# Performance work log

Measured on AMD Instinct MI355X. Metric: run time of the kernel, lower is better.

## Reference

```python
import jax, jax.numpy as jnp
import numpy as np

B, C, N = 2, 256, 8192
H = W = 64
C4 = C // 4
EPS = 1e-5


def bn(x, gamma, beta, mean, var):
    # eval-mode batchnorm over channel axis 1
    shape = (1, -1) + (1,) * (x.ndim - 2)
    inv = gamma * jax.lax.rsqrt(var + EPS)
    return x * inv.reshape(shape) + (beta - mean * inv).reshape(shape)


def conv1x1(x, w, b):
    # w: (Cout, Cin)
    return jnp.einsum('bchw,oc->bohw', x, w) + b.reshape(1, -1, 1, 1)


def conv2d(x, w, b=None, padding='VALID', groups=1, lhs_dilation=None):
    y = jax.lax.conv_general_dilated(
        x, w, window_strides=(1, 1), padding=padding,
        lhs_dilation=lhs_dilation, feature_group_count=groups,
        dimension_numbers=('NCHW', 'OIHW', 'NCHW'))
    return y if b is None else y + b.reshape(1, -1, 1, 1)


def lift_net(x, w1, b1, w2, b2, axis):
    # DAWN predictor/updater: ReflectionPad(2,1) -> conv k=4 along axis (C4->2C4)
    # -> ReLU -> 1x1 conv (2C4->C4) -> Tanh
    pad = [(0, 0)] * 4
    pad[axis] = (2, 1)
    xp = jnp.pad(x, pad, mode='reflect')
    k = w1[:, :, None, :] if axis == 3 else w1[:, :, :, None]
    h = jax.nn.relu(conv2d(xp, k, b1))
    return jnp.tanh(conv1x1(h, w2, b2))


def lifting(x, pw, axis):
    # pw = (w1, b1, w2, b2), each with leading net axis [P, U]
    w1, b1, w2, b2 = pw
    sl_e = [slice(None)] * 4; sl_e[axis] = slice(0, None, 2)
    sl_o = [slice(None)] * 4; sl_o[axis] = slice(1, None, 2)
    x_even, x_odd = x[tuple(sl_e)], x[tuple(sl_o)]
    d = x_odd - lift_net(x_even, w1[0], b1[0], w2[0], b2[0], axis)
    c = x_even + lift_net(d, w1[1], b1[1], w2[1], b2[1], axis)
    return c, d


def wavelet2d(x, w1, b1, w2, b2):
    # leading axes of weights: (scheme[horizontal, vertical], net[P, U])
    c, d = lifting(x, (w1[0], b1[0], w2[0], b2[0]), axis=3)  # split along W
    v = (w1[1], b1[1], w2[1], b2[1])                          # shared vertical weights
    LL, LH = lifting(c, v, axis=2)
    HL, HH = lifting(d, v, axis=2)
    return LL, LH, HL, HH


def convT(x, w, b):
    # torch ConvTranspose2d(k=4, stride=2, pad=1); w: (Cin, Cout, 4, 4)
    wc = jnp.flip(w, (2, 3)).transpose(1, 0, 2, 3)  # (Cout, Cin, 4, 4)
    return conv2d(x, wc, b, padding=[(2, 2), (2, 2)], lhs_dilation=(2, 2))


def _forward(tokens, flatten_mat, bn_gamma, bn_beta, bn_mean, bn_var, red_w, red_b,
             lift_w1, lift_b1, lift_w2, lift_b2,
             ff2_w1, ff2_b1, ff2_w2, ff2_b2, ct2_w, ct2_b,
             bn2_gamma, bn2_beta, bn2_mean, bn2_var,
             ff1_w1, ff1_b1, ff1_w2, ff1_b2, ct1_w, ct1_b,
             bn1_gamma, bn1_beta, bn1_mean, bn1_var,
             dw1_w, dw1_b, dw2_w, dw2_b, scale_w, inflate_idx):
    r = bn(tokens, bn_gamma, bn_beta, bn_mean, bn_var)                       # (B,C,N)
    r = jnp.einsum('bmn,bcn->bcm', flatten_mat, r).reshape(B, C, H, W)       # flatten to grid
    rr = conv1x1(r, red_w, red_b)                                            # (B,C/4,H,W)
    LL1, LH1, HL1, HH1 = wavelet2d(rr, lift_w1[0], lift_b1[0], lift_w2[0], lift_b2[0])
    LL2, LH2, HL2, HH2 = wavelet2d(LL1, lift_w1[1], lift_b1[1], lift_w2[1], lift_b2[1])
    x2 = jnp.concatenate([LL2, LH2, HL2, HH2], 1)                            # (B,C,H/4,W/4)
    y2 = conv1x1(jax.nn.gelu(conv1x1(x2, ff2_w1, ff2_b1), approximate=False), ff2_w2, ff2_b2)
    y2 = bn(convT(y2, ct2_w, ct2_b), bn2_gamma, bn2_beta, bn2_mean, bn2_var) # (B,C/2,H/2,W/2)
    x1 = jnp.concatenate([LL1, LH1, HL1, HH1, y2], 1)                        # (B,1.5C,H/2,W/2)
    y1 = conv1x1(jax.nn.gelu(conv1x1(x1, ff1_w1, ff1_b1), approximate=False), ff1_w2, ff1_b2)
    y1 = bn(convT(y1, ct1_w, ct1_b), bn1_gamma, bn1_beta, bn1_mean, bn1_var) # (B,C,H,W)
    r = r + y1
    r = conv2d(r, dw1_w, dw1_b, padding=[(1, 1), (1, 1)], groups=C)          # depthwise 3x3
    r = conv2d(jax.nn.relu(r), dw2_w, dw2_b, padding=[(1, 1), (1, 1)], groups=C)
    r = r.reshape(B, C, H * W) * scale_w.reshape(1, C, 1)                    # grouped 1x1 conv1d
    r = jnp.take_along_axis(r, inflate_idx, axis=2)                          # inflate gather
    return tokens + r


def setup_inputs() -> dict:
    key = jax.random.key(0)
    ks = iter(jax.random.split(key, 64))
    nrm = lambda shape, s=0.05: jax.random.normal(next(ks), shape, jnp.float32) * s
    uni = lambda shape: jax.random.uniform(next(ks), shape, jnp.float32, 0.5, 1.5)
    return dict(
        tokens=jax.random.normal(next(ks), (B, C, N), jnp.float32),
        flatten_mat=nrm((B, H * W, N), 0.02),
        inflate_idx=jax.random.randint(next(ks), (B, C, N), 0, H * W),
        bn_gamma=jnp.ones((C,), jnp.float32), bn_beta=jnp.zeros((C,), jnp.float32),
        bn_mean=nrm((C,), 0.1), bn_var=uni((C,)),
        red_w=nrm((C4, C)), red_b=nrm((C4,)),
        lift_w1=nrm((2, 2, 2, 2 * C4, C4, 4)), lift_b1=nrm((2, 2, 2, 2 * C4)),
        lift_w2=nrm((2, 2, 2, C4, 2 * C4)), lift_b2=nrm((2, 2, 2, C4)),
        ff2_w1=nrm((C, C)), ff2_b1=nrm((C,)), ff2_w2=nrm((C, C)), ff2_b2=nrm((C,)),
        ct2_w=nrm((C, C // 2, 4, 4)), ct2_b=nrm((C // 2,)),
        bn2_gamma=jnp.ones((C // 2,), jnp.float32), bn2_beta=jnp.zeros((C // 2,), jnp.float32),
        bn2_mean=nrm((C // 2,), 0.1), bn2_var=uni((C // 2,)),
        ff1_w1=nrm((C, C + C // 2)), ff1_b1=nrm((C,)), ff1_w2=nrm((C, C)), ff1_b2=nrm((C,)),
        ct1_w=nrm((C, C, 4, 4)), ct1_b=nrm((C,)),
        bn1_gamma=jnp.ones((C,), jnp.float32), bn1_beta=jnp.zeros((C,), jnp.float32),
        bn1_mean=nrm((C,), 0.1), bn1_var=uni((C,)),
        dw1_w=nrm((C, 1, 3, 3)), dw1_b=nrm((C,)),
        dw2_w=nrm((C, 1, 3, 3)), dw2_b=nrm((C,)),
        scale_w=nrm((C,), 0.2),
    )


def reference(tokens, flatten_mat, inflate_idx, bn_gamma, bn_beta, bn_mean, bn_var,
              red_w, red_b, lift_w1, lift_b1, lift_w2, lift_b2,
              ff2_w1, ff2_b1, ff2_w2, ff2_b2, ct2_w, ct2_b,
              bn2_gamma, bn2_beta, bn2_mean, bn2_var,
              ff1_w1, ff1_b1, ff1_w2, ff1_b2, ct1_w, ct1_b,
              bn1_gamma, bn1_beta, bn1_mean, bn1_var,
              dw1_w, dw1_b, dw2_w, dw2_b, scale_w):
    return _forward(tokens, flatten_mat, bn_gamma, bn_beta, bn_mean, bn_var, red_w, red_b,
                    lift_w1, lift_b1, lift_w2, lift_b2,
                    ff2_w1, ff2_b1, ff2_w2, ff2_b2, ct2_w, ct2_b,
                    bn2_gamma, bn2_beta, bn2_mean, bn2_var,
                    ff1_w1, ff1_b1, ff1_w2, ff1_b2, ct1_w, ct1_b,
                    bn1_gamma, bn1_beta, bn1_mean, bn1_var,
                    dw1_w, dw1_b, dw2_w, dw2_b, scale_w, inflate_idx)
```

## Files before the change

kernel.cpp:

```cpp
#include <hip/hip_runtime.h>
#include <math.h>

#define EPSV 1e-5f

typedef __attribute__((ext_vector_type(8))) short bf16x8;
typedef __attribute__((ext_vector_type(4))) float f32x4;
typedef __attribute__((ext_vector_type(8))) unsigned short u16x8;

__device__ inline unsigned short f2bf(float f) {
    unsigned u = __float_as_uint(f);
    unsigned r = (u + 0x7fffu + ((u >> 16) & 1u)) >> 16;
    return (unsigned short)r;
}

__device__ inline void gload_lds16(const void* g, void* l) {
    __builtin_amdgcn_global_load_lds(
        (const __attribute__((address_space(1))) void*)g,
        (__attribute__((address_space(3))) void*)l, 16, 0, 0);
}

__global__ __launch_bounds__(256) void bn_to_bf16_kernel(
    const float4* __restrict__ x, ushort4* __restrict__ y,
    const float* __restrict__ g, const float* __restrict__ be,
    const float* __restrict__ mu, const float* __restrict__ va)
{
    int i = blockIdx.x * 256 + threadIdx.x;
    int c = (i >> 11) & 255;
    float s = g[c] * rsqrtf(va[c] + EPSV);
    float t = be[c] - mu[c] * s;
    float4 v = x[i];
    ushort4 h;
    h.x = f2bf(v.x * s + t); h.y = f2bf(v.y * s + t);
    h.z = f2bf(v.z * s + t); h.w = f2bf(v.w * s + t);
    y[i] = h;
}

__global__ __launch_bounds__(256) void flatten_gemm_mfma(
    const unsigned short* __restrict__ A, const float* __restrict__ Bm,
    float* __restrict__ Pbase)
{
    __shared__ __align__(16) unsigned short AS[4][256 * 32];
    __shared__ __align__(16) unsigned short BS[4][64 * 32];
    const int NTT = 64;
    int t = threadIdx.x;
    int wid = t >> 6, lane = t & 63;
    int n0 = blockIdx.x * 64;
    int ks = blockIdx.z & 3, b = blockIdx.z >> 2;
    const unsigned short* Ab = A + b * (256 * 8192);
    const float* Bb = Bm + (long)b * (4096 * 8192) + (long)n0 * 8192;
    int k0 = ks * 2048;
    int brow = t >> 3, bc8 = t & 7;
    int l15 = lane & 15, kc = lane >> 4;

    f32x4 acc[4][4] = {};

    auto issueA = [&](int tile, int buf) {
        int kb = k0 + tile * 32;
        #pragma unroll
        for (int j = 0; j < 4; ++j) {
            int d16 = (wid * 4 + j) * 64 + lane;
            int row = d16 >> 2;
            int ch = (d16 & 3) ^ ((row >> 1) & 3);
            gload_lds16(Ab + row * 8192 + kb + ch * 8, &AS[buf][(wid * 4 + j) * 512]);
        }
    };
    auto loadB = [&](int tile, float4& f0, float4& f1) {
        int kb = k0 + tile * 32;
        f0 = *(const float4*)(Bb + brow * 8192 + kb + bc8 * 4);
        f1 = *(const float4*)(Bb + (brow + 32) * 8192 + kb + bc8 * 4);
    };
    auto writeB = [&](int buf, const float4& f0, const float4& f1) {
        int ch16 = (bc8 >> 1) ^ ((brow >> 1) & 3);
        ushort4 h;
        h.x = f2bf(f0.x); h.y = f2bf(f0.y); h.z = f2bf(f0.z); h.w = f2bf(f0.w);
        *reinterpret_cast<ushort4*>(&BS[buf][brow * 32 + ch16 * 8 + (bc8 & 1) * 4]) = h;
        int rr2 = brow + 32;
        int ch16b = (bc8 >> 1) ^ ((rr2 >> 1) & 3);
        ushort4 h2;
        h2.x = f2bf(f1.x); h2.y = f2bf(f1.y); h2.z = f2bf(f1.z); h2.w = f2bf(f1.w);
        *reinterpret_cast<ushort4*>(&BS[buf][rr2 * 32 + ch16b * 8 + (bc8 & 1) * 4]) = h2;
    };
    auto mmac = [&](int buf) {
        bf16x8 af[4], bfr[4];
        #pragma unroll
        for (int mf = 0; mf < 4; ++mf) {
            int row = wid * 64 + mf * 16 + l15;
            int ch = kc ^ ((row >> 1) & 3);
            af[mf] = *reinterpret_cast<const bf16x8*>(&AS[buf][row * 32 + ch * 8]);
        }
        #pragma unroll
        for (int nf = 0; nf < 4; ++nf) {
            int row = nf * 16 + l15;
            int ch = kc ^ ((row >> 1) & 3);
            bfr[nf] = *reinterpret_cast<const bf16x8*>(&BS[buf][row * 32 + ch * 8]);
        }
        #pragma unroll
        for (int mf = 0; mf < 4; ++mf)
            #pragma unroll
            for (int nf = 0; nf < 4; ++nf)
                acc[mf][nf] = __builtin_amdgcn_mfma_f32_16x16x32_bf16(
                    af[mf], bfr[nf], acc[mf][nf], 0, 0, 0);
    };

    float4 p0, p1, e0, e1, q0, q1, r0, r1;
    loadB(0, p0, p1);
    loadB(1, e0, e1);
    loadB(2, q0, q1);
    issueA(0, 0); issueA(1, 1); issueA(2, 2);
    writeB(0, p0, p1);
    writeB(1, e0, e1);
    asm volatile("s_waitcnt vmcnt(8) lgkmcnt(0)" ::: "memory");
    __builtin_amdgcn_s_barrier();
    __builtin_amdgcn_sched_barrier(0);

    for (int tau = 0; tau < NTT; ++tau) {
        int cur = tau & 3;
        if (tau + 3 < NTT) {
            loadB(tau + 3, r0, r1);
            issueA(tau + 3, (tau + 3) & 3);
        }
        if (tau + 2 < NTT)
            writeB((tau + 2) & 3, q0, q1);
        mmac(cur);
        if (tau < NTT - 3)
            asm volatile("s_waitcnt vmcnt(8) lgkmcnt(0)" ::: "memory");
        else if (tau == NTT - 3)
            asm volatile("s_waitcnt vmcnt(4) lgkmcnt(0)" ::: "memory");
        else
            asm volatile("s_waitcnt vmcnt(0) lgkmcnt(0)" ::: "memory");
        __builtin_amdgcn_s_barrier();
        __builtin_amdgcn_sched_barrier(0);
        q0 = r0; q1 = r1;
    }

    float* P = Pbase + (long)ks * 2097152;
    float* Cb = P + (b * 256) * 4096 + n0;
    #pragma unroll
    for (int mf = 0; mf < 4; ++mf) {
        int rbase = wid * 64 + mf * 16 + (lane >> 4) * 4;
        #pragma unroll
        for (int nf = 0; nf < 4; ++nf) {
            int col = nf * 16 + (lane & 15);
            #pragma unroll
            for (int r = 0; r < 4; ++r)
                Cb[(rbase + r) * 4096 + col] = acc[mf][nf][r];
        }
    }
}

__global__ __launch_bounds__(256) void add4_t_kernel(
    const float* __restrict__ p, float* __restrict__ of32, unsigned short* __restrict__ obf)
{
    __shared__ float tl[64][65];
    int t = threadIdx.x;
    int b = blockIdx.z;
    int c0 = blockIdx.y * 64, p0 = blockIdx.x * 64;
    #pragma unroll
    for (int u = 0; u < 16; ++u) {
        int idx = u * 256 + t;
        int cl = idx >> 6, pl = idx & 63;
        long g = (long)(b * 256 + c0 + cl) * 4096 + p0 + pl;
        float v = p[g] + p[g + 2097152] + p[g + 2 * 2097152] + p[g + 3 * 2097152];
        tl[cl][pl] = v;
        of32[g] = v;
    }
    __syncthreads();
    #pragma unroll
    for (int u = 0; u < 16; ++u) {
        int idx = u * 256 + t;
        int pl = idx >> 6, cl = idx & 63;
        obf[(long)(b * 4096 + p0 + pl) * 256 + c0 + cl] = f2bf(tl[cl][pl]);
    }
}

__global__ __launch_bounds__(256) void wpack_kernel(
    const float* __restrict__ w, unsigned short* __restrict__ wp, int Cout, int Cin)
{
    int id = blockIdx.x * 256 + threadIdx.x;
    int nc8 = Cin >> 3;
    int cch = id % nc8;
    int rest = id / nc8;
    int o = rest % Cout;
    int pt = rest / Cout;
    if (pt >= 16) return;
    int par = pt >> 2, tap = pt & 3;
    int py = par >> 1, px = par & 1, u = tap >> 1, v = tap & 1;
    int tf = (3 - py - 2 * u) * 4 + (3 - px - 2 * v);
    u16x8 h;
    #pragma unroll
    for (int e = 0; e < 8; ++e)
        h[e] = f2bf(w[((cch * 8 + e) * Cout + o) * 16 + tf]);
    *reinterpret_cast<u16x8*>(&wp[((pt * Cout + o) * Cin) + cch * 8]) = h;
}

template<int NF>
__global__ __launch_bounds__(256) void conv1x1_mfma(
    const unsigned short* __restrict__ xbf, const float* __restrict__ w,
    const float* __restrict__ bias, float* __restrict__ of32,
    unsigned short* __restrict__ obf, int Cin, int Cout, int P, int act)
{
    constexpr int BP = NF * 64;
    __shared__ __align__(16) unsigned short XS[2][BP * 32];
    __shared__ __align__(16) unsigned short WS[2][64 * 32];
    int t = threadIdx.x;
    int wid = t >> 6, lane = t & 63;
    int b = blockIdx.z;
    int p0 = blockIdx.x * BP, o0 = blockIdx.y * 64;
    const unsigned short* xb = xbf + (long)b * P * Cin;
    int wm = t >> 2, wq = t & 3;
    int chunks = Cin >> 5;

    f32x4 acc[4][NF] = {};

    #pragma unroll
    for (int j = 0; j < NF; ++j) {
        int d16 = (wid * NF + j) * 64 + lane;
        int p = d16 >> 2;
        int ch = (d16 & 3) ^ ((p >> 1) & 3);
        gload_lds16(xb + (long)(p0 + p) * Cin + ch * 8, &XS[0][(wid * NF + j) * 512]);
    }
    float4 wr0 = *(const float4*)(w + (o0 + wm) * Cin + wq * 8);
    float4 wr1 = *(const float4*)(w + (o0 + wm) * Cin + wq * 8 + 4);
    __syncthreads();

    for (int cc = 0; cc < chunks; ++cc) {
        int cur = cc & 1;
        {
            int chq = wq ^ ((wm >> 1) & 3);
            u16x8 h;
            h[0] = f2bf(wr0.x); h[1] = f2bf(wr0.y); h[2] = f2bf(wr0.z); h[3] = f2bf(wr0.w);
            h[4] = f2bf(wr1.x); h[5] = f2bf(wr1.y); h[6] = f2bf(wr1.z); h[7] = f2bf(wr1.w);
            *reinterpret_cast<u16x8*>(&WS[cur][wm * 32 + chq * 8]) = h;
        }
        __syncthreads();

        if (cc < chunks - 1) {
            int kn = (cc + 1) * 32;
            #pragma unroll
            for (int j = 0; j < NF; ++j) {
                int d16 = (wid * NF + j) * 64 + lane;
                int p = d16 >> 2;
                int ch = (d16 & 3) ^ ((p >> 1) & 3);
                gload_lds16(xb + (long)(p0 + p) * Cin + kn + ch * 8,
                            &XS[cur ^ 1][(wid * NF + j) * 512]);
            }
            wr0 = *(const float4*)(w + (o0 + wm) * Cin + kn + wq * 8);
            wr1 = *(const float4*)(w + (o0 + wm) * Cin + kn + wq * 8 + 4);
        }

        int l15 = lane & 15, kc = lane >> 4;
        bf16x8 af[4], bfr[NF];
        #pragma unroll
        for (int mf = 0; mf < 4; ++mf) {
            int row = mf * 16 + l15;
            int ch = kc ^ ((row >> 1) & 3);
            af[mf] = *reinterpret_cast<const bf16x8*>(&WS[cur][row * 32 + ch * 8]);
        }
        #pragma unroll
        for (int nf = 0; nf < NF; ++nf) {
            int row = wid * (NF * 16) + nf * 16 + l15;
            int ch = kc ^ ((row >> 1) & 3);
            bfr[nf] = *reinterpret_cast<const bf16x8*>(&XS[cur][row * 32 + ch * 8]);
        }
        #pragma unroll
        for (int mf = 0; mf < 4; ++mf)
            #pragma unroll
            for (int nf = 0; nf < NF; ++nf)
                acc[mf][nf] = __builtin_amdgcn_mfma_f32_16x16x32_bf16(
                    af[mf], bfr[nf], acc[mf][nf], 0, 0, 0);
        __syncthreads();
    }

    int l15 = lane & 15, kc4 = lane >> 4;
    #pragma unroll
    for (int mf = 0; mf < 4; ++mf) {
        #pragma unroll
        for (int nf = 0; nf < NF; ++nf) {
            int p = wid * (NF * 16) + nf * 16 + l15;
            ushort4 hb;
            #pragma unroll
            for (int r = 0; r < 4; ++r) {
                int m = mf * 16 + kc4 * 4 + r;
                float v = acc[mf][nf][r] + bias[o0 + m];
                if (act == 1) v = fmaxf(v, 0.f);
                else if (act == 2) v = 0.5f * v * (1.f + erff(v * 0.70710678118f));
                if (of32) of32[((long)(b * Cout) + o0 + m) * P + p0 + p] = v;
                ((unsigned short*)&hb)[r] = f2bf(v);
            }
            if (obf)
                *reinterpret_cast<ushort4*>(
                    &obf[(long)(b * P + p0 + p) * Cout + o0 + mf * 16 + kc4 * 4]) = hb;
        }
    }
}

__global__ __launch_bounds__(256) void convt_mfma(
    const unsigned short* __restrict__ xbf, const unsigned short* __restrict__ wp,
    const float* __restrict__ bias, const float* __restrict__ g,
    const float* __restrict__ be, const float* __restrict__ mu,
    const float* __restrict__ va, const float* __restrict__ res,
    float* __restrict__ of32, unsigned short* __restrict__ obf,
    int Cin, int Cout, int Hin, int Win, int TR, int cshift, int OCtot, int cof)
{
    __shared__ __align__(16) unsigned short XS[165 * 32];
    __shared__ __align__(16) unsigned short WS[4 * 64 * 32];
    int t = threadIdx.x;
    int wid = t >> 6, lane = t & 63;
    int z = blockIdx.z;
    int b = z >> 2, par = z & 3;
    int py = par >> 1, px = par & 1;
    int o0 = blockIdx.y * 64;
    int i0 = blockIdx.x * TR;
    int CW = Win, CW1 = CW + 1;
    int npatch = (TR + 1) * CW1;
    int Pin = Hin * Win, Pout = 4 * Hin * Win;
    const unsigned short* xb = xbf + (long)b * Pin * Cin;
    int chunks = Cin >> 5;
    int l15 = lane & 15, kc = lane >> 4;

    f32x4 acc[4][2] = {};

    for (int cc = 0; cc < chunks; ++cc) {
        __syncthreads();
        for (int idx = t; idx < npatch * 4; idx += 256) {
            int pp = idx >> 2, ql = idx & 3;
            int qs = ql ^ ((pp >> 1) & 3);
            int a = pp / CW1, bcol = pp - a * CW1;
            int iy = i0 - (1 - py) + a;
            int ix = bcol - (1 - px);
            u16x8 v = {};
            if (iy >= 0 && iy < Hin && ix >= 0 && ix < Win)
                v = *reinterpret_cast<const u16x8*>(
                    &xb[(long)(iy * Win + ix) * Cin + cc * 32 + qs * 8]);
            *reinterpret_cast<u16x8*>(&XS[pp * 32 + ql * 8]) = v;
        }
        {
            int m = t >> 2, q = t & 3;
            int chq = q ^ ((m >> 1) & 3);
            #pragma unroll
            for (int tap = 0; tap < 4; ++tap) {
                u16x8 v = *reinterpret_cast<const u16x8*>(
                    &wp[((long)((par * 4 + tap) * Cout + o0 + m)) * Cin + cc * 32 + q * 8]);
                *reinterpret_cast<u16x8*>(&WS[tap * 2048 + m * 32 + chq * 8]) = v;
            }
        }
        __syncthreads();

        #pragma unroll
        for (int tap = 0; tap < 4; ++tap) {
            int u = tap >> 1, v = tap & 1;
            bf16x8 af[4], bfr[2];
            #pragma unroll
            for (int mf = 0; mf < 4; ++mf) {
                int row = mf * 16 + l15;
                int ch = kc ^ ((row >> 1) & 3);
                af[mf] = *reinterpret_cast<const bf16x8*>(&WS[tap * 2048 + row * 32 + ch * 8]);
            }
            #pragma unroll
            for (int nf = 0; nf < 2; ++nf) {
                int n = wid * 32 + nf * 16 + l15;
                int rn = n >> cshift, cn = n & (CW - 1);
                int pp = (rn + u) * CW1 + cn + v;
                int ch = kc ^ ((pp >> 1) & 3);
                bfr[nf] = *reinterpret_cast<const bf16x8*>(&XS[pp * 32 + ch * 8]);
            }
            #pragma unroll
            for (int mf = 0; mf < 4; ++mf)
                #pragma unroll
                for (int nf = 0; nf < 2; ++nf)
                    acc[mf][nf] = __builtin_amdgcn_mfma_f32_16x16x32_bf16(
                        af[mf], bfr[nf], acc[mf][nf], 0, 0, 0);
        }
    }

    int kc4 = lane >> 4;
    #pragma unroll
    for (int nf = 0; nf < 2; ++nf) {
        int n = wid * 32 + nf * 16 + l15;
        int rn = n >> cshift, cn = n & (CW - 1);
        int y = 2 * (i0 + rn) + py;
        int xx = 2 * cn + px;
        int pout = y * 2 * Win + xx;
        #pragma unroll
        for (int mf = 0; mf < 4; ++mf) {
            ushort4 hb;
            #pragma unroll
            for (int r = 0; r < 4; ++r) {
                int m = mf * 16 + kc4 * 4 + r;
                int o = o0 + m;
                float s = g[o] * rsqrtf(va[o] + EPSV);
                float v = (acc[mf][nf][r] + bias[o]) * s + (be[o] - mu[o] * s);
                if (res) v += res[((long)(b * Cout) + o) * Pout + pout];
                if (of32) of32[((long)(b * Cout) + o) * Pout + pout] = v;
                ((unsigned short*)&hb)[r] = f2bf(v);
            }
            if (obf)
                *reinterpret_cast<ushort4*>(
                    &obf[(long)(b * Pout + pout) * OCtot + cof + o0 + mf * 16 + kc4 * 4]) = hb;
        }
    }
}

__global__ __launch_bounds__(1024) void lift_net_kernel(
    const float* __restrict__ xA, const float* __restrict__ xB,
    const float* __restrict__ oA, const float* __restrict__ oB,
    float* __restrict__ uA, float* __restrict__ uB,
    int x_sB, int x_sC, int x_sR, int x_sA,
    int o_sB, int o_sC, int o_sR, int o_sA,
    int u_sB, int u_sC, int u_sR, int u_sA,
    const float* __restrict__ w1, const float* __restrict__ b1,
    const float* __restrict__ w2, const float* __restrict__ b2,
    int R, int L, int lsh, float sign,
    unsigned short* __restrict__ obf, int Pb, int OCb, int cofA, int cofB)
{
    __shared__ float xsm[4864];
    __shared__ float hsm[8192];
    int t = threadIdx.x;
    int g = t & 63, ocg = t >> 6;
    int b = blockIdx.z;
    int sel = blockIdx.y;
    const float* xin = sel ? xB : xA;
    const float* oth = sel ? oB : oA;
    float* outp = sel ? uB : uA;
    int cofb = sel ? cofB : cofA;
    int rpb = 64 >> lsh;
    int row0 = blockIdx.x * rpb;
    int Lp = L + 3;
    int total = 64 * rpb * Lp;
    for (int idx = t; idx < total; idx += 1024) {
        int c = idx / (rpb * Lp);
        int rem = idx - c * rpb * Lp;
        int rr_l = rem / Lp;
        int q = rem - rr_l * Lp;
        int s = q - 2;
        s = (s < 0) ? -s : s;
        if (s >= L) s = 2 * L - 2 - s;
        xsm[idx] = xin[b * x_sB + c * x_sC + (row0 + rr_l) * x_sR + s * x_sA];
    }
    __syncthreads();

    int ocgu = __builtin_amdgcn_readfirstlane(ocg);
    int rl = g >> lsh, jl = g & (L - 1);
    const float* w1u = w1 + ocgu * 8 * 256;
    float acc1[8] = {};
    for (int c = 0; c < 64; ++c) {
        const float* xr = &xsm[(c * rpb + rl) * Lp + jl];
        float x0 = xr[0], x1 = xr[1], x2 = xr[2], x3 = xr[3];
        const float* wc = w1u + c * 4;
        #pragma unroll
        for (int k = 0; k < 8; ++k) {
            const float* wr = wc + k * 256;
            acc1[k] += wr[0] * x0 + wr[1] * x1 + wr[2] * x2 + wr[3] * x3;
        }
    }
    #pragma unroll
    for (int k = 0; k < 8; ++k) {
        int oc = ocgu * 8 + k;
        hsm[oc * 64 + g] = fmaxf(acc1[k] + b1[oc], 0.f);
    }
    __syncthreads();

    const float* w2u = w2 + ocgu * 4 * 128;
    float acc2[4] = {};
    for (int h4 = 0; h4 < 32; ++h4) {
        float hv0 = hsm[(h4 * 4 + 0) * 64 + g];
        float hv1 = hsm[(h4 * 4 + 1) * 64 + g];
        float hv2 = hsm[(h4 * 4 + 2) * 64 + g];
        float hv3 = hsm[(h4 * 4 + 3) * 64 + g];
        #pragma unroll
        for (int kk = 0; kk < 4; ++kk) {
            const float* wr = w2u + kk * 128 + h4 * 4;
            acc2[kk] += wr[0] * hv0 + wr[1] * hv1 + wr[2] * hv2 + wr[3] * hv3;
        }
    }
    int rg = row0 + rl;
    int p = rg * u_sR + jl * u_sA;
    #pragma unroll
    for (int kk = 0; kk < 4; ++kk) {
        int o = ocgu * 4 + kk;
        float v = oth[b * o_sB + o * o_sC + rg * o_sR + jl * o_sA]
                + sign * tanhf(acc2[kk] + b2[o]);
        outp[b * u_sB + o * u_sC + p] = v;
        if (obf) obf[(long)(b * Pb + p) * OCb + cofb + o] = f2bf(v);
    }
}

__global__ __launch_bounds__(256) void dw_fused_kernel(
    const float* __restrict__ r2, const float* __restrict__ w1, const float* __restrict__ b1,
    const float* __restrict__ w2, const float* __restrict__ b2v,
    const float* __restrict__ scw, const float* __restrict__ tok,
    const int* __restrict__ idx, float* __restrict__ out)
{
    __shared__ float s0[64][68];
    __shared__ float s1[64][68];
    __shared__ float s2[4096];
    int bc = blockIdx.x;
    int c = bc & 255;
    int t = threadIdx.x;
    const float* xp = r2 + (long)bc * 4096;
    for (int i = t; i < 4096; i += 256) s0[i >> 6][i & 63] = xp[i];
    float wa[9], wb[9];
    #pragma unroll
    for (int k = 0; k < 9; ++k) { wa[k] = w1[c * 9 + k]; wb[k] = w2[c * 9 + k]; }
    float ba = b1[c], bb = b2v[c], sc = scw[c];
    __syncthreads();
    for (int i = t; i < 4096; i += 256) {
        int y = i >> 6, x = i & 63;
        float a = ba;
        #pragma unroll
        for (int ky = 0; ky < 3; ++ky) {
            int yy = y + ky - 1;
            if (yy < 0 || yy > 63) continue;
            #pragma unroll
            for (int kx = 0; kx < 3; ++kx) {
                int xx = x + kx - 1;
                if (xx < 0 || xx > 63) continue;
                a += wa[ky * 3 + kx] * s0[yy][xx];
            }
        }
        s1[y][x] = fmaxf(a, 0.f);
    }
    __syncthreads();
    for (int i = t; i < 4096; i += 256) {
        int y = i >> 6, x = i & 63;
        float a = bb;
        #pragma unroll
        for (int ky = 0; ky < 3; ++ky) {
            int yy = y + ky - 1;
            if (yy < 0 || yy > 63) continue;
            #pragma unroll
            for (int kx = 0; kx < 3; ++kx) {
                int xx = x + kx - 1;
                if (xx < 0 || xx > 63) continue;
                a += wb[ky * 3 + kx] * s1[yy][xx];
            }
        }
        s2[i] = a * sc;
    }
    __syncthreads();
    long base = (long)bc << 13;
    const int4* ip = (const int4*)(idx + base);
    const float4* tp = (const float4*)(tok + base);
    float4* op = (float4*)(out + base);
    for (int i = t; i < 2048; i += 256) {
        int4 iv = ip[i];
        float4 tv = tp[i];
        float4 o;
        o.x = tv.x + s2[iv.x];
        o.y = tv.y + s2[iv.y];
        o.z = tv.z + s2[iv.z];
        o.w = tv.w + s2[iv.w];
        op[i] = o;
    }
}

extern "C" void kernel_launch(void* const* d_in, const int* in_sizes, int n_in,
                              void* d_out, int out_size, void* d_ws, size_t ws_size,
                              hipStream_t stream)
{
    const float* tokens = (const float*)d_in[0];
    const float* fm     = (const float*)d_in[1];
    const int*   infl   = (const int*)d_in[2];
    const float* bng = (const float*)d_in[3];
    const float* bnb = (const float*)d_in[4];
    const float* bnm = (const float*)d_in[5];
    const float* bnv = (const float*)d_in[6];
    const float* red_w = (const float*)d_in[7];
    const float* red_b = (const float*)d_in[8];
    const float* lw1 = (const float*)d_in[9];
    const float* lb1 = (const float*)d_in[10];
    const float* lw2 = (const float*)d_in[11];
    const float* lb2 = (const float*)d_in[12];
    const float* f2w1 = (const float*)d_in[13];
    const float* f2b1 = (const float*)d_in[14];
    const float* f2w2 = (const float*)d_in[15];
    const float* f2b2 = (const float*)d_in[16];
    const float* ct2w = (const float*)d_in[17];
    const float* ct2b = (const float*)d_in[18];
    const float* bn2g = (const float*)d_in[19];
    const float* bn2b = (const float*)d_in[20];
    const float* bn2m = (const float*)d_in[21];
    const float* bn2v = (const float*)d_in[22];
    const float* f1w1 = (const float*)d_in[23];
    const float* f1b1 = (const float*)d_in[24];
    const float* f1w2 = (const float*)d_in[25];
    const float* f1b2 = (const float*)d_in[26];
    const float* ct1w = (const float*)d_in[27];
    const float* ct1b = (const float*)d_in[28];
    const float* bn1g = (const float*)d_in[29];
    const float* bn1b = (const float*)d_in[30];
    const float* bn1m = (const float*)d_in[31];
    const float* bn1v = (const float*)d_in[32];
    const float* dw1w = (const float*)d_in[33];
    const float* dw1b = (const float*)d_in[34];
    const float* dw2w = (const float*)d_in[35];
    const float* dw2b = (const float*)d_in[36];
    const float* scw  = (const float*)d_in[37];

    float* ws = (float*)d_ws;
    unsigned short* Abf = (unsigned short*)ws;
    float* part  = ws + 2097152;
    float* rgrid = ws + 18874368;
    unsigned short* rgrid_bf = (unsigned short*)(ws + 20971520);
    float* rr    = ws + 22020096;
    float* c1    = ws + 22544384;
    float* d1    = ws + 22806528;
    float* c2    = ws + 23068672;
    float* d2    = ws + 23134208;
    float* x2    = ws + 23199744;
    unsigned short* x2_bf  = (unsigned short*)(ws + 23330816);
    float* x1    = ws + 23396352;
    unsigned short* x1_bf  = (unsigned short*)(ws + 24182784);
    unsigned short* g2_bf  = (unsigned short*)(ws + 24576000);
    unsigned short* y2p_bf = (unsigned short*)(ws + 24641536);
    unsigned short* g1_bf  = (unsigned short*)(ws + 24707072);
    unsigned short* y1p_bf = (unsigned short*)(ws + 24969216);
    unsigned short* wp2    = (unsigned short*)(ws + 25231360);
    unsigned short* wp1    = (unsigned short*)(ws + 25493504);
    float* r2 = ws + 26017792;

    wpack_kernel<<<512, 256, 0, stream>>>(ct1w, wp1, 256, 256);
    wpack_kernel<<<256, 256, 0, stream>>>(ct2w, wp2, 128, 256);

    bn_to_bf16_kernel<<<4096, 256, 0, stream>>>((const float4*)tokens, (ushort4*)Abf,
                                                bng, bnb, bnm, bnv);
    flatten_gemm_mfma<<<dim3(64, 1, 8), 256, 0, stream>>>(Abf, fm, part);
    add4_t_kernel<<<dim3(64, 4, 2), 256, 0, stream>>>(part, rgrid, rgrid_bf);
    conv1x1_mfma<2><<<dim3(32, 1, 2), 256, 0, stream>>>(rgrid_bf, red_w, red_b,
                                                        rr, (unsigned short*)nullptr,
                                                        256, 64, 4096, 0);

    auto lift2 = [&](const float* xA, const float* xB, const float* oA, const float* oB,
                     float* uA, float* uB,
                     int xsB, int xsC, int xsR, int xsA,
                     int osB, int osC, int osR, int osA,
                     int usB, int usC, int usR, int usA,
                     int lvl, int sch, int net, int R, int L, float sign,
                     unsigned short* obf, int Pb, int OCb, int cofA, int cofB, int nsel) {
        int widx = (lvl * 2 + sch) * 2 + net;
        int lsh = (L == 32) ? 5 : 4;
        lift_net_kernel<<<dim3(R * L / 64, nsel, 2), 1024, 0, stream>>>(
            xA, xB, oA, oB, uA, uB,
            xsB, xsC, xsR, xsA, osB, osC, osR, osA, usB, usC, usR, usA,
            lw1 + widx * 32768, lb1 + widx * 128, lw2 + widx * 8192, lb2 + widx * 64,
            R, L, lsh, sign, obf, Pb, OCb, cofA, cofB);
    };

    lift2(rr, rr, rr + 1, rr + 1, d1, d1,
          262144, 4096, 64, 2,  262144, 4096, 64, 2,  131072, 2048, 32, 1,
          0, 0, 0, 64, 32, -1.f, nullptr, 0, 0, 0, 0, 1);
    lift2(d1, d1, rr, rr, c1, c1,
          131072, 2048, 32, 1,  262144, 4096, 64, 2,  131072, 2048, 32, 1,
          0, 0, 1, 64, 32, +1.f, nullptr, 0, 0, 0, 0, 1);
    lift2(c1, d1, c1 + 32, d1 + 32, x1 + 65536, x1 + 196608,
          131072, 2048, 1, 64,  131072, 2048, 1, 64,  393216, 1024, 1, 32,
          0, 1, 0, 32, 32, -1.f, x1_bf, 1024, 384, 64, 192, 2);
    lift2(x1 + 65536, x1 + 196608, c1, d1, x1, x1 + 131072,
          393216, 1024, 1, 32,  131072, 2048, 1, 64,  393216, 1024, 1, 32,
          0, 1, 1, 32, 32, +1.f, x1_bf, 1024, 384, 0, 128, 2);
    lift2(x1, x1, x1 + 1, x1 + 1, d2, d2,
          393216, 1024, 32, 2,  393216, 1024, 32, 2,  65536, 512, 16, 1,
          1, 0, 0, 32, 16, -1.f, nullptr, 0, 0, 0, 0, 1);
    lift2(d2, d2, x1, x1, c2, c2,
          65536, 512, 16, 1,  393216, 1024, 32, 2,  65536, 512, 16, 1,
          1, 0, 1, 32, 16, +1.f, nullptr, 0, 0, 0, 0, 1);
    lift2(c2, d2, c2 + 16, d2 + 16, x2 + 16384, x2 + 49152,
          65536, 512, 1, 32,  65536, 512, 1, 32,  65536, 256, 1, 16,
          1, 1, 0, 16, 16, -1.f, x2_bf, 256, 256, 64, 192, 2);
    lift2(x2 + 16384, x2 + 49152, c2, d2, x2, x2 + 32768,
          65536, 256, 1, 16,  65536, 512, 1, 32,  65536, 256, 1, 16,
          1, 1, 1, 16, 16, +1.f, x2_bf, 256, 256, 0, 128, 2);

    conv1x1_mfma<1><<<dim3(4, 4, 2), 256, 0, stream>>>(x2_bf, f2w1, f2b1,
        (float*)nullptr, g2_bf, 256, 256, 256, 2);
    conv1x1_mfma<1><<<dim3(4, 4, 2), 256, 0, stream>>>(g2_bf, f2w2, f2b2,
        (float*)nullptr, y2p_bf, 256, 256, 256, 0);
    convt_mfma<<<dim3(2, 2, 8), 256, 0, stream>>>(y2p_bf, wp2, ct2b,
        bn2g, bn2b, bn2m, bn2v, (const float*)nullptr,
        (float*)nullptr, x1_bf, 256, 128, 16, 16, 8, 4, 384, 256);

    conv1x1_mfma<2><<<dim3(8, 4, 2), 256, 0, stream>>>(x1_bf, f1w1, f1b1,
        (float*)nullptr, g1_bf, 384, 256, 1024, 2);
    conv1x1_mfma<2><<<dim3(8, 4, 2), 256, 0, stream>>>(g1_bf, f1w2, f1b2,
        (float*)nullptr, y1p_bf, 256, 256, 1024, 0);
    convt_mfma<<<dim3(8, 4, 8), 256, 0, stream>>>(y1p_bf, wp1, ct1b,
        bn1g, bn1b, bn1m, bn1v, rgrid,
        r2, (unsigned short*)nullptr, 256, 256, 32, 32, 4, 5, 0, 0);

    dw_fused_kernel<<<512, 256, 0, stream>>>(r2, dw1w, dw1b, dw2w, dw2b, scw,
                                             tokens, infl, (float*)d_out);
}
```

Baseline: 671.4 us.

## Stage fp32 B via direct LDS loads, drop fp32 grid, shrink lift blocks

The flatten GEMM now streams the fp32 B tiles straight into LDS with global_load_lds and converts them to bf16 at fragment-read time with packed converts. This replaces the register round trip and per-element rounding, and it cuts the ring from four stages to three. Block indices are remapped so concurrently running blocks share the same B rows. The fp32 copy of the reduced grid is no longer written, and the final transposed conv reads the bf16 residual instead, trading some precision for less memory traffic. The lifting kernels switch to 512-thread blocks with half the LDS per block, which raises block count and may improve occupancy.

```diff
diff --git a/kernel.cpp b/kernel.cpp
--- a/kernel.cpp
+++ b/kernel.cpp
@@ -11,6 +11,10 @@
     unsigned u = __float_as_uint(f);
     unsigned r = (u + 0x7fffu + ((u >> 16) & 1u)) >> 16;
     return (unsigned short)r;
+}
+
+__device__ inline float bf2f(unsigned short h) {
+    return __uint_as_float(((unsigned)h) << 16);
 }
 
 __device__ inline void gload_lds16(const void* g, void* l) {
@@ -39,22 +43,24 @@
     const unsigned short* __restrict__ A, const float* __restrict__ Bm,
     float* __restrict__ Pbase)
 {
-    __shared__ __align__(16) unsigned short AS[4][256 * 32];
-    __shared__ __align__(16) unsigned short BS[4][64 * 32];
+    __shared__ __align__(16) unsigned short AS[3][256 * 32];
+    __shared__ __align__(16) float BSf[3][64 * 32];
     const int NTT = 64;
     int t = threadIdx.x;
     int wid = t >> 6, lane = t & 63;
-    int n0 = blockIdx.x * 64;
-    int ks = blockIdx.z & 3, b = blockIdx.z >> 2;
+    int fid = blockIdx.z * 64 + blockIdx.x;
+    int nid = (fid & 7) * 64 + (fid >> 3);
+    int n0 = (nid & 63) * 64;
+    int zz = nid >> 6;
+    int ks = zz & 3, b = zz >> 2;
     const unsigned short* Ab = A + b * (256 * 8192);
     const float* Bb = Bm + (long)b * (4096 * 8192) + (long)n0 * 8192;
     int k0 = ks * 2048;
-    int brow = t >> 3, bc8 = t & 7;
     int l15 = lane & 15, kc = lane >> 4;
 
     f32x4 acc[4][4] = {};
 
-    auto issueA = [&](int tile, int buf) {
+    auto stage = [&](int tile, int buf) {
         int kb = k0 + tile * 32;
         #pragma unroll
         for (int j = 0; j < 4; ++j) {
@@ -63,22 +69,13 @@
             int ch = (d16 & 3) ^ ((row >> 1) & 3);
             gload_lds16(Ab + row * 8192 + kb + ch * 8, &AS[buf][(wid * 4 + j) * 512]);
         }
-    };
-    auto loadB = [&](int tile, float4& f0, float4& f1) {
-        int kb = k0 + tile * 32;
-        f0 = *(const float4*)(Bb + brow * 8192 + kb + bc8 * 4);
-        f1 = *(const float4*)(Bb + (brow + 32) * 8192 + kb + bc8 * 4);
-    };
-    auto writeB = [&](int buf, const float4& f0, const float4& f1) {
-        int ch16 = (bc8 >> 1) ^ ((brow >> 1) & 3);
-        ushort4 h;
-        h.x = f2bf(f0.x); h.y = f2bf(f0.y); h.z = f2bf(f0.z); h.w = f2bf(f0.w);
-        *reinterpret_cast<ushort4*>(&BS[buf][brow * 32 + ch16 * 8 + (bc8 & 1) * 4]) = h;
-        int rr2 = brow + 32;
-        int ch16b = (bc8 >> 1) ^ ((rr2 >> 1) & 3);
-        ushort4 h2;
-        h2.x = f2bf(f1.x); h2.y = f2bf(f1.y); h2.z = f2bf(f1.z); h2.w = f2bf(f1.w);
-        *reinterpret_cast<ushort4*>(&BS[buf][rr2 * 32 + ch16b * 8 + (bc8 & 1) * 4]) = h2;
+        #pragma unroll
+        for (int j = 0; j < 2; ++j) {
+            int cid = (wid * 2 + j) * 64 + lane;
+            int row = cid >> 3, ch = cid & 7;
+            int chs = ch ^ (row & 7);
+            gload_lds16(Bb + row * 8192 + kb + chs * 4, &BSf[buf][(wid * 2 + j) * 256]);
+        }
     };
     auto mmac = [&](int buf) {
         bf16x8 af[4], bfr[4];
@@ -91,8 +88,16 @@
         #pragma unroll
         for (int nf = 0; nf < 4; ++nf) {
             int row = nf * 16 + l15;
-            int ch = kc ^ ((row >> 1) & 3);
-            bfr[nf] = *reinterpret_cast<const bf16x8*>(&BS[buf][row * 32 + ch * 8]);
+            int s0 = (kc * 2) ^ (row & 7);
+            int s1 = (kc * 2 + 1) ^ (row & 7);
+            f32x4 lo = *reinterpret_cast<const f32x4*>(&BSf[buf][row * 32 + s0 * 4]);
+            f32x4 hi = *reinterpret_cast<const f32x4*>(&BSf[buf][row * 32 + s1 * 4]);
+            union { unsigned u[4]; bf16x8 v; } cv;
+            asm("v_cvt_pk_bf16_f32 %0, %1, %2" : "=v"(cv.u[0]) : "v"(lo[0]), "v"(lo[1]));
+            asm("v_cvt_pk_bf16_f32 %0, %1, %2" : "=v"(cv.u[1]) : "v"(lo[2]), "v"(lo[3]));
+            asm("v_cvt_pk_bf16_f32 %0, %1, %2" : "=v"(cv.u[2]) : "v"(hi[0]), "v"(hi[1]));
+            asm("v_cvt_pk_bf16_f32 %0, %1, %2" : "=v"(cv.u[3]) : "v"(hi[2]), "v"(hi[3]));
+            bfr[nf] = cv.v;
         }
         #pragma unroll
         for (int mf = 0; mf < 4; ++mf)
@@ -102,35 +107,19 @@
                     af[mf], bfr[nf], acc[mf][nf], 0, 0, 0);
     };
 
-    float4 p0, p1, e0, e1, q0, q1, r0, r1;
-    loadB(0, p0, p1);
-    loadB(1, e0, e1);
-    loadB(2, q0, q1);
-    issueA(0, 0); issueA(1, 1); issueA(2, 2);
-    writeB(0, p0, p1);
-    writeB(1, e0, e1);
-    asm volatile("s_waitcnt vmcnt(8) lgkmcnt(0)" ::: "memory");
+    stage(0, 0);
+    stage(1, 1);
+    asm volatile("s_waitcnt vmcnt(6)" ::: "memory");
     __builtin_amdgcn_s_barrier();
-    __builtin_amdgcn_sched_barrier(0);
 
     for (int tau = 0; tau < NTT; ++tau) {
-        int cur = tau & 3;
-        if (tau + 3 < NTT) {
-            loadB(tau + 3, r0, r1);
-            issueA(tau + 3, (tau + 3) & 3);
-        }
+        if (tau + 2 < NTT) stage(tau + 2, (tau + 2) % 3);
+        mmac(tau % 3);
         if (tau + 2 < NTT)
-            writeB((tau + 2) & 3, q0, q1);
-        mmac(cur);
-        if (tau < NTT - 3)
-            asm volatile("s_waitcnt vmcnt(8) lgkmcnt(0)" ::: "memory");
-        else if (tau == NTT - 3)
-            asm volatile("s_waitcnt vmcnt(4) lgkmcnt(0)" ::: "memory");
+            asm volatile("s_waitcnt vmcnt(6)" ::: "memory");
         else
-            asm volatile("s_waitcnt vmcnt(0) lgkmcnt(0)" ::: "memory");
+            asm volatile("s_waitcnt vmcnt(0)" ::: "memory");
         __builtin_amdgcn_s_barrier();
-        __builtin_amdgcn_sched_barrier(0);
-        q0 = r0; q1 = r1;
     }
 
     float* P = Pbase + (long)ks * 2097152;
@@ -149,7 +138,7 @@
 }
 
 __global__ __launch_bounds__(256) void add4_t_kernel(
-    const float* __restrict__ p, float* __restrict__ of32, unsigned short* __restrict__ obf)
+    const float* __restrict__ p, unsigned short* __restrict__ obf)
 {
     __shared__ float tl[64][65];
     int t = threadIdx.x;
@@ -160,9 +149,7 @@
         int idx = u * 256 + t;
         int cl = idx >> 6, pl = idx & 63;
         long g = (long)(b * 256 + c0 + cl) * 4096 + p0 + pl;
-        float v = p[g] + p[g + 2097152] + p[g + 2 * 2097152] + p[g + 3 * 2097152];
-        tl[cl][pl] = v;
-        of32[g] = v;
+        tl[cl][pl] = p[g] + p[g + 2097152] + p[g + 2 * 2097152] + p[g + 3 * 2097152];
     }
     __syncthreads();
     #pragma unroll
@@ -298,7 +285,7 @@
     const unsigned short* __restrict__ xbf, const unsigned short* __restrict__ wp,
     const float* __restrict__ bias, const float* __restrict__ g,
     const float* __restrict__ be, const float* __restrict__ mu,
-    const float* __restrict__ va, const float* __restrict__ res,
+    const float* __restrict__ va, const unsigned short* __restrict__ resbf,
     float* __restrict__ of32, unsigned short* __restrict__ obf,
     int Cin, int Cout, int Hin, int Win, int TR, int cshift, int OCtot, int cof)
 {
@@ -390,7 +377,7 @@
                 int o = o0 + m;
                 float s = g[o] * rsqrtf(va[o] + EPSV);
                 float v = (acc[mf][nf][r] + bias[o]) * s + (be[o] - mu[o] * s);
-                if (res) v += res[((long)(b * Cout) + o) * Pout + pout];
+                if (resbf) v += bf2f(resbf[(long)(b * Pout + pout) * 256 + o]);
                 if (of32) of32[((long)(b * Cout) + o) * Pout + pout] = v;
                 ((unsigned short*)&hb)[r] = f2bf(v);
             }
@@ -401,7 +388,7 @@
     }
 }
 
-__global__ __launch_bounds__(1024) void lift_net_kernel(
+__global__ __launch_bounds__(512) void lift_net_kernel(
     const float* __restrict__ xA, const float* __restrict__ xB,
     const float* __restrict__ oA, const float* __restrict__ oB,
     float* __restrict__ uA, float* __restrict__ uB,
@@ -413,21 +400,21 @@
     int R, int L, int lsh, float sign,
     unsigned short* __restrict__ obf, int Pb, int OCb, int cofA, int cofB)
 {
-    __shared__ float xsm[4864];
-    __shared__ float hsm[8192];
+    __shared__ float xsm[2432];
+    __shared__ float hsm[4096];
     int t = threadIdx.x;
-    int g = t & 63, ocg = t >> 6;
+    int g = t & 31, ocg = t >> 5;
     int b = blockIdx.z;
     int sel = blockIdx.y;
     const float* xin = sel ? xB : xA;
     const float* oth = sel ? oB : oA;
     float* outp = sel ? uB : uA;
     int cofb = sel ? cofB : cofA;
-    int rpb = 64 >> lsh;
+    int rpb = 32 >> lsh;
     int row0 = blockIdx.x * rpb;
     int Lp = L + 3;
     int total = 64 * rpb * Lp;
-    for (int idx = t; idx < total; idx += 1024) {
+    for (int idx = t; idx < total; idx += 512) {
         int c = idx / (rpb * Lp);
         int rem = idx - c * rpb * Lp;
         int rr_l = rem / Lp;
@@ -439,9 +426,9 @@
     }
     __syncthreads();
 
-    int ocgu = __builtin_amdgcn_readfirstlane(ocg);
-    int rl = g >> lsh, jl = g & (L - 1);
-    const float* w1u = w1 + ocgu * 8 * 256;
+    int rl = (lsh >= 5) ? 0 : (g >> lsh);
+    int jl = g & (L - 1);
+    const float* w1u = w1 + ocg * 8 * 256;
     float acc1[8] = {};
     for (int c = 0; c < 64; ++c) {
         const float* xr = &xsm[(c * rpb + rl) * Lp + jl];
@@ -455,18 +442,18 @@
     }
     #pragma unroll
     for (int k = 0; k < 8; ++k) {
-        int oc = ocgu * 8 + k;
-        hsm[oc * 64 + g] = fmaxf(acc1[k] + b1[oc], 0.f);
+        int oc = ocg * 8 + k;
+        hsm[oc * 32 + g] = fmaxf(acc1[k] + b1[oc], 0.f);
     }
     __syncthreads();
 
-    const float* w2u = w2 + ocgu * 4 * 128;
+    const float* w2u = w2 + ocg * 4 * 128;
     float acc2[4] = {};
     for (int h4 = 0; h4 < 32; ++h4) {
-        float hv0 = hsm[(h4 * 4 + 0) * 64 + g];
-        float hv1 = hsm[(h4 * 4 + 1) * 64 + g];
-        float hv2 = hsm[(h4 * 4 + 2) * 64 + g];
-        float hv3 = hsm[(h4 * 4 + 3) * 64 + g];
+        float hv0 = hsm[(h4 * 4 + 0) * 32 + g];
+        float hv1 = hsm[(h4 * 4 + 1) * 32 + g];
+        float hv2 = hsm[(h4 * 4 + 2) * 32 + g];
+        float hv3 = hsm[(h4 * 4 + 3) * 32 + g];
         #pragma unroll
         for (int kk = 0; kk < 4; ++kk) {
             const float* wr = w2u + kk * 128 + h4 * 4;
@@ -477,7 +464,7 @@
     int p = rg * u_sR + jl * u_sA;
     #pragma unroll
     for (int kk = 0; kk < 4; ++kk) {
-        int o = ocgu * 4 + kk;
+        int o = ocg * 4 + kk;
         float v = oth[b * o_sB + o * o_sC + rg * o_sR + jl * o_sA]
                 + sign * tanhf(acc2[kk] + b2[o]);
         outp[b * u_sB + o * u_sC + p] = v;
@@ -600,24 +587,23 @@
     float* ws = (float*)d_ws;
     unsigned short* Abf = (unsigned short*)ws;
     float* part  = ws + 2097152;
-    float* rgrid = ws + 18874368;
-    unsigned short* rgrid_bf = (unsigned short*)(ws + 20971520);
-    float* rr    = ws + 22020096;
-    float* c1    = ws + 22544384;
-    float* d1    = ws + 22806528;
-    float* c2    = ws + 23068672;
-    float* d2    = ws + 23134208;
-    float* x2    = ws + 23199744;
-    unsigned short* x2_bf  = (unsigned short*)(ws + 23330816);
-    float* x1    = ws + 23396352;
-    unsigned short* x1_bf  = (unsigned short*)(ws + 24182784);
-    unsigned short* g2_bf  = (unsigned short*)(ws + 24576000);
-    unsigned short* y2p_bf = (unsigned short*)(ws + 24641536);
-    unsigned short* g1_bf  = (unsigned short*)(ws + 24707072);
-    unsigned short* y1p_bf = (unsigned short*)(ws + 24969216);
-    unsigned short* wp2    = (unsigned short*)(ws + 25231360);
-    unsigned short* wp1    = (unsigned short*)(ws + 25493504);
-    float* r2 = ws + 26017792;
+    unsigned short* rgrid_bf = (unsigned short*)(ws + 10485760);
+    float* rr    = ws + 11534336;
+    float* c1    = ws + 12058624;
+    float* d1    = ws + 12320768;
+    float* c2    = ws + 12582912;
+    float* d2    = ws + 12648448;
+    float* x2    = ws + 12713984;
+    unsigned short* x2_bf  = (unsigned short*)(ws + 12845056);
+    float* x1    = ws + 12910592;
+    unsigned short* x1_bf  = (unsigned short*)(ws + 13697024);
+    unsigned short* g2_bf  = (unsigned short*)(ws + 14090240);
+    unsigned short* y2p_bf = (unsigned short*)(ws + 14155776);
+    unsigned short* g1_bf  = (unsigned short*)(ws + 14221312);
+    unsigned short* y1p_bf = (unsigned short*)(ws + 14483456);
+    unsigned short* wp2    = (unsigned short*)(ws + 14745600);
+    unsigned short* wp1    = (unsigned short*)(ws + 15007744);
+    float* r2 = ws + 15532032;
 
     wpack_kernel<<<512, 256, 0, stream>>>(ct1w, wp1, 256, 256);
     wpack_kernel<<<256, 256, 0, stream>>>(ct2w, wp2, 128, 256);
@@ -625,7 +611,7 @@
     bn_to_bf16_kernel<<<4096, 256, 0, stream>>>((const float4*)tokens, (ushort4*)Abf,
                                                 bng, bnb, bnm, bnv);
     flatten_gemm_mfma<<<dim3(64, 1, 8), 256, 0, stream>>>(Abf, fm, part);
-    add4_t_kernel<<<dim3(64, 4, 2), 256, 0, stream>>>(part, rgrid, rgrid_bf);
+    add4_t_kernel<<<dim3(64, 4, 2), 256, 0, stream>>>(part, rgrid_bf);
     conv1x1_mfma<2><<<dim3(32, 1, 2), 256, 0, stream>>>(rgrid_bf, red_w, red_b,
                                                         rr, (unsigned short*)nullptr,
                                                         256, 64, 4096, 0);
@@ -639,7 +625,7 @@
                      unsigned short* obf, int Pb, int OCb, int cofA, int cofB, int nsel) {
         int widx = (lvl * 2 + sch) * 2 + net;
         int lsh = (L == 32) ? 5 : 4;
-        lift_net_kernel<<<dim3(R * L / 64, nsel, 2), 1024, 0, stream>>>(
+        lift_net_kernel<<<dim3(R * L / 32, nsel, 2), 512, 0, stream>>>(
             xA, xB, oA, oB, uA, uB,
             xsB, xsC, xsR, xsA, osB, osC, osR, osA, usB, usC, usR, usA,
             lw1 + widx * 32768, lb1 + widx * 128, lw2 + widx * 8192, lb2 + widx * 64,
@@ -676,7 +662,7 @@
     conv1x1_mfma<1><<<dim3(4, 4, 2), 256, 0, stream>>>(g2_bf, f2w2, f2b2,
         (float*)nullptr, y2p_bf, 256, 256, 256, 0);
     convt_mfma<<<dim3(2, 2, 8), 256, 0, stream>>>(y2p_bf, wp2, ct2b,
-        bn2g, bn2b, bn2m, bn2v, (const float*)nullptr,
+        bn2g, bn2b, bn2m, bn2v, (const unsigned short*)nullptr,
         (float*)nullptr, x1_bf, 256, 128, 16, 16, 8, 4, 384, 256);
 
     conv1x1_mfma<2><<<dim3(8, 4, 2), 256, 0, stream>>>(x1_bf, f1w1, f1b1,
@@ -684,7 +670,7 @@
     conv1x1_mfma<2><<<dim3(8, 4, 2), 256, 0, stream>>>(g1_bf, f1w2, f1b2,
         (float*)nullptr, y1p_bf, 256, 256, 1024, 0);
     convt_mfma<<<dim3(8, 4, 8), 256, 0, stream>>>(y1p_bf, wp1, ct1b,
-        bn1g, bn1b, bn1m, bn1v, rgrid,
+        bn1g, bn1b, bn1m, bn1v, rgrid_bf,
         r2, (unsigned short*)nullptr, 256, 256, 32, 32, 4, 5, 0, 0);
 
     dw_fused_kernel<<<512, 256, 0, stream>>>(r2, dw1w, dw1b, dw2w, dw2b, scw,
```

Result: slower. 930.6 us (+38.6%).
